# Kernel tuning notes

Hardware: AMD Instinct MI355X
Metric: run time of the kernel (lower is better)

Reference implementation:

```python
import jax, jax.numpy as jnp
import numpy as np

D = 1024
H = 16
DH = D // H
L = 128  # max_pos_len
B = 4
T = 1024
SCALE = float(np.sqrt(D / H))


def setup_inputs() -> dict:
    key = jax.random.key(0)
    ks = jax.random.split(key, 9)
    x_q = jax.random.normal(ks[0], (B, T, D), dtype=jnp.float32)
    x_k = jax.random.normal(ks[1], (B, T, D), dtype=jnp.float32)
    x_v = jax.random.normal(ks[2], (B, T, D), dtype=jnp.float32)
    mask = jax.random.randint(ks[3], (B, 1, 1, T), 0, 2) == 1  # bool, True = masked
    Wq = jax.random.normal(ks[4], (D, D), dtype=jnp.float32) * 0.02
    Wk = jax.random.normal(ks[5], (D, D), dtype=jnp.float32) * 0.02
    Wv = jax.random.normal(ks[6], (D, D), dtype=jnp.float32) * 0.02
    Wo = jax.random.normal(ks[7], (D, D), dtype=jnp.float32) * 0.02
    pos_emb = jax.random.normal(ks[8], (2 * L + 1, DH), dtype=jnp.float32)
    return {"x_q": x_q, "x_k": x_k, "x_v": x_v, "mask": mask,
            "Wq": Wq, "Wk": Wk, "Wv": Wv, "Wo": Wo, "pos_emb": pos_emb}


def reference(x_q, x_k, x_v, mask, Wq, Wk, Wv, Wo, pos_emb):
    # nn.Linear(bias=False): y = x @ W.T
    def split_heads(x):  # (B,T,D) -> (B,H,T,DH)
        return x.reshape(B, -1, H, DH).transpose(0, 2, 1, 3)

    Q = split_heads(x_q @ Wq.T)
    K = split_heads(x_k @ Wk.T)
    V = split_heads(x_v @ Wv.T)

    logits = jnp.einsum('bhqd,bhkd->bhqk', Q, K)

    # arrange_char_pos_embedding: indices[q,k] = clamp(k-q, -L, L) + L
    rel = jnp.clip(jnp.arange(T)[None, :] - jnp.arange(T)[:, None], -L, L) + L
    arranged_pos = pos_emb[rel]  # (T_Q, T_K, DH)
    pos_logits = jnp.einsum('bhqd,qkd->bhqk', Q, arranged_pos)

    logits = (logits + pos_logits) / SCALE
    logits = jnp.where(mask, -jnp.inf, logits)  # mask broadcasts (B,1,1,T)
    attn = jax.nn.softmax(logits, axis=-1)  # dropout p=0.0 -> identity

    combined = jnp.einsum('bhqk,bhkd->bhqd', attn, V)
    heads_concat = combined.transpose(0, 2, 1, 3).reshape(B, -1, D)
    return heads_concat @ Wo.T
```

## Files before the change

### kernel.cpp

```cpp
#include <hip/hip_runtime.h>
#include <hip/hip_bf16.h>
#include <stdint.h>

typedef __attribute__((ext_vector_type(8))) short short8;
typedef __attribute__((ext_vector_type(4))) float f32x4;

__device__ __forceinline__ uint16_t f2bf(float f) {
    union { float f; uint32_t u; } v; v.f = f;
    uint32_t r = v.u + 0x7FFF + ((v.u >> 16) & 1);
    return (uint16_t)(r >> 16);
}
__device__ __forceinline__ float bf2f(uint16_t u) {
    union { uint32_t u; float f; } v; v.u = ((uint32_t)u) << 16;
    return v.f;
}
__device__ __forceinline__ float exp2_raw(float x) {
    float r;
    asm("v_exp_f32 %0, %1" : "=v"(r) : "v"(x));
    return r;
}
__device__ __forceinline__ uint32_t cvt_pk_bf16(float lo, float hi) {
    uint32_t r;
    asm("v_cvt_pk_bf16_f32 %0, %1, %2" : "=v"(r) : "v"(lo), "v"(hi));
    return r;
}

template<int F32>
__device__ __forceinline__ uint4 load8(const void* p, size_t off) {
    if (F32) {
        const float* f = (const float*)p + off;
        float4 f0 = *(const float4*)f;
        float4 f1 = *(const float4*)(f + 4);
        uint4 r;
        r.x = (uint32_t)f2bf(f0.x) | ((uint32_t)f2bf(f0.y) << 16);
        r.y = (uint32_t)f2bf(f0.z) | ((uint32_t)f2bf(f0.w) << 16);
        r.z = (uint32_t)f2bf(f1.x) | ((uint32_t)f2bf(f1.y) << 16);
        r.w = (uint32_t)f2bf(f1.z) | ((uint32_t)f2bf(f1.w) << 16);
        return r;
    } else {
        return *(const uint4*)((const uint16_t*)p + off);
    }
}

#define GLDS(gp, lp) __builtin_amdgcn_global_load_lds( \
    (const __attribute__((address_space(1))) void*)(gp), \
    (__attribute__((address_space(3))) void*)(lp), 16, 0, 0)

struct CvtSeg { const float* s; uint16_t* d; int n8; };
struct CvtArgs {
    CvtSeg seg[9]; int nseg;
    const void* mraw; unsigned long long* mbits; uint16_t* mvals;
};

__global__ __launch_bounds__(256) void cvt_bf16(CvtArgs a)
{
    if (blockIdx.x == 0) {
        __shared__ int flags[3];
        __shared__ uint8_t mloc[4096];
        const uint32_t* w = (const uint32_t*)a.mraw;
        const uint8_t* b8 = (const uint8_t*)a.mraw;
        const int t = threadIdx.x;
        if (t < 3) flags[t] = 0;
        __syncthreads();
        int fbyte = 0, ff32 = 0, fodd = 0;
        for (int i = t; i < 1024; i += 256) {
            uint32_t v = w[i];
            if (v != 0u && v != 1u && v != 0x3F800000u) fbyte = 1;
            if (v == 0x3F800000u) ff32 = 1;
            if ((i & 1) && v != 0u) fodd = 1;
        }
        if (fbyte) atomicOr(&flags[0], 1);
        if (ff32)  atomicOr(&flags[1], 1);
        if (fodd)  atomicOr(&flags[2], 1);
        __syncthreads();
        int mode;
        if (flags[0]) mode = 1;
        else if (flags[1]) mode = 0;
        else if (!flags[2]) mode = 2;
        else mode = 0;
        for (int k = t; k < 4096; k += 256) {
            int val;
            if (mode == 1)      val = (b8[k] != 0);
            else if (mode == 2) val = (w[2 * k] != 0u);
            else                val = (w[k] != 0u);
            mloc[k] = (uint8_t)val;
        }
        __syncthreads();
        for (int k = t; k < 4096; k += 256)
            a.mvals[k] = mloc[k] ? (uint16_t)0 : (uint16_t)0x3F80;
        if (t < 64) {
            uint64_t bits = 0;
#pragma unroll
            for (int i = 0; i < 64; ++i)
                bits |= (uint64_t)mloc[t * 64 + i] << i;
            a.mbits[t] = bits;
        }
    }
    const int tid = blockIdx.x * 256 + threadIdx.x;
    const int stride = gridDim.x * 256;
    for (int s = 0; s < a.nseg; ++s) {
        const float* src = a.seg[s].s;
        uint16_t* dst = a.seg[s].d;
        const int n8 = a.seg[s].n8;
        if (src) {
            for (int i = tid; i < n8; i += stride)
                *(uint4*)(dst + (size_t)i * 8) = load8<1>(src, (size_t)i * 8);
        } else {
            const uint4 z = {0u, 0u, 0u, 0u};
            for (int i = tid; i < n8; i += stride)
                *(uint4*)(dst + (size_t)i * 8) = z;
        }
    }
}

__global__ __launch_bounds__(256) void gemm128_qkv(
    const uint16_t* __restrict__ xq, const uint16_t* __restrict__ xk, const uint16_t* __restrict__ xv,
    const uint16_t* __restrict__ Wq, const uint16_t* __restrict__ Wk, const uint16_t* __restrict__ Wv,
    uint16_t* __restrict__ Qh, uint16_t* __restrict__ Khd, uint16_t* __restrict__ Vt,
    const unsigned long long* __restrict__ mbits)
{
    __shared__ alignas(16) uint16_t As[2][128 * 32];
    __shared__ alignas(16) uint16_t Bs[2][128 * 32];

    const int z = blockIdx.z;
    const uint16_t* A = (z == 0) ? xq : (z == 1) ? xk : xv;
    const uint16_t* B = (z == 0) ? Wq : (z == 1) ? Wk : Wv;
    uint16_t* C = (z == 0) ? Qh : (z == 1) ? Khd : Vt;
    const int cm = (z == 2) ? 2 : 1;
    const int bm = blockIdx.x, bn = blockIdx.y;
    const int K = 1024;

    const int t = threadIdx.x;
    const int lane = t & 63, wave = t >> 6;
    const int lrow = lane & 15, quad = lane >> 4;
    const int wr = (wave >> 1) * 64, wc = (wave & 1) * 64;
    const int g_row = wave * 16 + (lane >> 2);
    const int g_col = (lane & 3) * 8;

    const f32x4 fz = {0.f, 0.f, 0.f, 0.f};
    f32x4 acc[4][4];
#pragma unroll
    for (int i = 0; i < 4; ++i)
#pragma unroll
        for (int j = 0; j < 4; ++j) acc[i][j] = fz;

    for (int k0 = 0; k0 < K; k0 += 64) {
        __syncthreads();
#pragma unroll
        for (int kh = 0; kh < 2; ++kh) {
            const int kk = k0 + kh * 32;
            GLDS(A + (size_t)(bm * 128 + g_row) * K + kk + g_col,      As[kh] + wave * 512);
            GLDS(A + (size_t)(bm * 128 + g_row + 64) * K + kk + g_col, As[kh] + wave * 512 + 2048);
            GLDS(B + (size_t)(bn * 128 + g_row) * K + kk + g_col,      Bs[kh] + wave * 512);
            GLDS(B + (size_t)(bn * 128 + g_row + 64) * K + kk + g_col, Bs[kh] + wave * 512 + 2048);
        }
        __syncthreads();

#pragma unroll
        for (int kh = 0; kh < 2; ++kh) {
            short8 a[4], b[4];
#pragma unroll
            for (int i = 0; i < 4; ++i)
                a[i] = *(const short8*)(As[kh] + (wr + i * 16 + lrow) * 32 + quad * 8);
#pragma unroll
            for (int j = 0; j < 4; ++j)
                b[j] = *(const short8*)(Bs[kh] + (wc + j * 16 + lrow) * 32 + quad * 8);
#pragma unroll
            for (int i = 0; i < 4; ++i)
#pragma unroll
                for (int j = 0; j < 4; ++j)
                    acc[i][j] = __builtin_amdgcn_mfma_f32_16x16x32_bf16(a[i], b[j], acc[i][j], 0, 0, 0);
        }
    }

    if (cm == 2) {
        __syncthreads();
        uint16_t* scr = As[0] + wave * 1024;
#pragma unroll
        for (int i = 0; i < 4; ++i)
#pragma unroll
            for (int j = 0; j < 4; ++j) {
                uint2 pk;
                pk.x = (uint32_t)f2bf(acc[i][j][0]) | ((uint32_t)f2bf(acc[i][j][1]) << 16);
                pk.y = (uint32_t)f2bf(acc[i][j][2]) | ((uint32_t)f2bf(acc[i][j][3]) << 16);
                *(uint2*)(scr + lrow * 16 + quad * 4) = pk;
                if (lane < 32) {
                    int n = lane >> 1, m8 = (lane & 1) * 8;
                    short8 vv = *(const short8*)(scr + n * 16 + m8);
                    int ng = bn * 128 + wc + j * 16 + n;
                    int hh = ng >> 6, d = ng & 63;
                    int mg = bm * 128 + wr + i * 16;
                    int bb = mg >> 10, tl = (mg & 1023) + m8;
                    uint32_t eb = (uint32_t)(mbits[(size_t)bb * 16 + (tl >> 6)] >> (tl & 63)) & 0xFFu;
                    if (eb) {
                        union { short8 s; uint32_t u[4]; } uw;
                        uw.s = vv;
#pragma unroll
                        for (int c = 0; c < 4; ++c) {
                            uint32_t km = (((eb >> (2 * c)) & 1) ? 0u : 0x0000FFFFu)
                                        | (((eb >> (2 * c + 1)) & 1) ? 0u : 0xFFFF0000u);
                            uw.u[c] &= km;
                        }
                        vv = uw.s;
                    }
                    *(short8*)(C + ((((size_t)bb * 16 + hh) * 64 + d) * 1024 + tl)) = vv;
                }
            }
        return;
    }

#pragma unroll
    for (int i = 0; i < 4; ++i)
#pragma unroll
        for (int j = 0; j < 4; ++j)
#pragma unroll
            for (int r = 0; r < 4; ++r) {
                int m = bm * 128 + wr + i * 16 + quad * 4 + r;
                int n = bn * 128 + wc + j * 16 + lrow;
                int bb = m >> 10, tt = m & 1023, hh = n >> 6, d = n & 63;
                C[(((size_t)bb * 16 + hh) * 1024 + tt) * 64 + d] = f2bf(acc[i][j][r]);
            }
}

__global__ __launch_bounds__(256) void gemm_out(
    const uint16_t* __restrict__ A, const uint16_t* __restrict__ B,
    float* __restrict__ C, int M, int N, int K)
{
    __shared__ alignas(16) uint16_t As[2][64 * 32];
    __shared__ alignas(16) uint16_t Bs[2][128 * 32];

    const int t = threadIdx.x;
    const int lane = t & 63, wave = t >> 6;
    const int lrow = lane & 15, quad = lane >> 4;
    const int wr = (wave >> 1) * 32, wc = (wave & 1) * 64;
    const int g_row = wave * 16 + (lane >> 2);
    const int g_col = (lane & 3) * 8;
    const int bm = blockIdx.x, bn = blockIdx.y;

    const f32x4 fz = {0.f, 0.f, 0.f, 0.f};
    f32x4 acc[2][4];
#pragma unroll
    for (int i = 0; i < 2; ++i)
#pragma unroll
        for (int j = 0; j < 4; ++j) acc[i][j] = fz;

    for (int k0 = 0; k0 < K; k0 += 64) {
        __syncthreads();
#pragma unroll
        for (int kh = 0; kh < 2; ++kh) {
            const int kk = k0 + kh * 32;
            GLDS(A + (size_t)(bm * 64 + g_row) * K + kk + g_col,       As[kh] + wave * 512);
            GLDS(B + (size_t)(bn * 128 + g_row) * K + kk + g_col,      Bs[kh] + wave * 512);
            GLDS(B + (size_t)(bn * 128 + g_row + 64) * K + kk + g_col, Bs[kh] + wave * 512 + 2048);
        }
        __syncthreads();

#pragma unroll
        for (int kh = 0; kh < 2; ++kh) {
            short8 a[2], b[4];
#pragma unroll
            for (int i = 0; i < 2; ++i)
                a[i] = *(const short8*)(As[kh] + (wr + i * 16 + lrow) * 32 + quad * 8);
#pragma unroll
            for (int j = 0; j < 4; ++j)
                b[j] = *(const short8*)(Bs[kh] + (wc + j * 16 + lrow) * 32 + quad * 8);
#pragma unroll
            for (int i = 0; i < 2; ++i)
#pragma unroll
                for (int j = 0; j < 4; ++j)
                    acc[i][j] = __builtin_amdgcn_mfma_f32_16x16x32_bf16(a[i], b[j], acc[i][j], 0, 0, 0);
        }
    }

#pragma unroll
    for (int i = 0; i < 2; ++i)
#pragma unroll
        for (int j = 0; j < 4; ++j)
#pragma unroll
            for (int r = 0; r < 4; ++r) {
                int m = bm * 64 + wr + i * 16 + quad * 4 + r;
                int n = bn * 128 + wc + j * 16 + lrow;
                C[(size_t)m * N + n] = acc[i][j][r];
            }
}

__global__ __launch_bounds__(256) void flash_attn(
    const uint16_t* __restrict__ Qh, const uint16_t* __restrict__ Kh,
    const uint16_t* __restrict__ Vt, const uint16_t* __restrict__ pos,
    const uint16_t* __restrict__ maskv, uint16_t* __restrict__ comb)
{
    const int blk = blockIdx.x;
    const int jj = blk >> 3;
    const int bh = (blk & 7) * 8 + (jj >> 4);
    const int qt = jj & 15;
    const int b = bh >> 4;
    const int h = bh & 15;
    const int t = threadIdx.x;
    const int lane = t & 63;
    const int wave = t >> 6;
    const int lrow = lane & 15;
    const int quad = lane >> 4;
    const int qb = qt * 64 + wave * 16;

    __shared__ alignas(16) uint16_t Ks[2][4096];
    __shared__ alignas(16) uint16_t Vs[2][4096];
    __shared__ alignas(16) uint16_t Qpos_l[64][277];
    __shared__ alignas(16) uint16_t Pl[4][16][72];
    __shared__ alignas(16) uint16_t maskl[1024];

    const uint16_t* Kp = Kh + (size_t)bh * 65536;
    const uint16_t* Vp = Vt + (size_t)bh * 65536;

    const int sg_r = lane >> 2;
    const int sg_c = ((lane & 3) ^ ((sg_r >> 1) & 3)) * 8;
    const int hw = wave >> 1;
    const int gw = (wave & 1) * 2;
    const int rdc = (quad ^ ((lrow >> 1) & 3)) * 8;

    const float CS = 0.18033688011f;

#pragma unroll
    for (int gg = 0; gg < 2; ++gg) {
        int g = gw + gg;
        GLDS(Kp + (size_t)(g * 16 + sg_r) * 64 + hw * 32 + sg_c, &Ks[0][hw * 2048 + g * 512]);
        GLDS(Vp + (size_t)(g * 16 + sg_r) * 1024 + hw * 32 + sg_c, &Vs[0][hw * 2048 + g * 512]);
    }
    if (wave < 2)
        GLDS(maskv + (size_t)b * 1024 + wave * 512 + lane * 8, maskl + wave * 512);

    const uint16_t* Qp = Qh + ((size_t)bh * 1024 + qb) * 64;
    short8 aq0 = *(const short8*)(Qp + (size_t)lrow * 64 + quad * 8);
    short8 aq1 = *(const short8*)(Qp + (size_t)lrow * 64 + 32 + quad * 8);

    const f32x4 fz = {0.f, 0.f, 0.f, 0.f};

#pragma unroll 4
    for (int nt = 0; nt < 17; ++nt) {
        short8 pb0 = *(const short8*)(pos + (size_t)(nt * 16 + lrow) * 64 + quad * 8);
        short8 pb1 = *(const short8*)(pos + (size_t)(nt * 16 + lrow) * 64 + 32 + quad * 8);
        f32x4 c = __builtin_amdgcn_mfma_f32_16x16x32_bf16(aq0, pb0, fz, 0, 0, 0);
        c = __builtin_amdgcn_mfma_f32_16x16x32_bf16(aq1, pb1, c, 0, 0, 0);
        const uint32_t p01 = cvt_pk_bf16(c[0] * CS, c[1] * CS);
        const uint32_t p23 = cvt_pk_bf16(c[2] * CS, c[3] * CS);
        const int row = wave * 16 + quad * 4;
        const int col = nt * 16 + lrow;
        Qpos_l[row + 0][col] = (uint16_t)p01;
        Qpos_l[row + 1][col] = (uint16_t)(p01 >> 16);
        Qpos_l[row + 2][col] = (uint16_t)p23;
        Qpos_l[row + 3][col] = (uint16_t)(p23 >> 16);
    }

    float pcl[4], pch[4];
#pragma unroll
    for (int r = 0; r < 4; ++r) {
        int ql = wave * 16 + quad * 4 + r;
        pcl[r] = bf2f(Qpos_l[ql][0]);
        pch[r] = bf2f(Qpos_l[ql][256]);
    }

    f32x4 o[4] = {fz, fz, fz, fz};
    f32x4 lacc = fz;

    for (int kb = 0; kb < 1024; kb += 64) {
        const int cur = (kb >> 6) & 1;
        __syncthreads();
        if (kb + 64 < 1024) {
            const int nxt = cur ^ 1;
#pragma unroll
            for (int gg = 0; gg < 2; ++gg) {
                int g = gw + gg;
                GLDS(Kp + (size_t)(kb + 64 + g * 16 + sg_r) * 64 + hw * 32 + sg_c,
                     &Ks[nxt][hw * 2048 + g * 512]);
                GLDS(Vp + (size_t)(g * 16 + sg_r) * 1024 + kb + 64 + hw * 32 + sg_c,
                     &Vs[nxt][hw * 2048 + g * 512]);
            }
        }
        const uint16_t* Kc = Ks[cur];
        const uint16_t* Vc = Vs[cur];

        f32x4 s[4];
        __builtin_amdgcn_s_setprio(1);
#pragma unroll
        for (int j = 0; j < 4; ++j) {
            short8 k0 = *(const short8*)(Kc + (j * 16 + lrow) * 32 + rdc);
            short8 k1 = *(const short8*)(Kc + 2048 + (j * 16 + lrow) * 32 + rdc);
            s[j] = __builtin_amdgcn_mfma_f32_16x16x32_bf16(aq0, k0, fz, 0, 0, 0);
            s[j] = __builtin_amdgcn_mfma_f32_16x16x32_bf16(aq1, k1, s[j], 0, 0, 0);
        }
        __builtin_amdgcn_s_setprio(0);

        const int diff = kb - qb;
        if (diff <= -192 || diff >= 144) {
            const bool low = (diff <= -192);
#pragma unroll
            for (int j = 0; j < 4; ++j) {
                float e[4];
#pragma unroll
                for (int r = 0; r < 4; ++r) {
                    float pc = low ? pcl[r] : pch[r];
                    e[r] = exp2_raw(__builtin_fmaf(s[j][r], CS, pc));
                }
                const uint32_t p01 = cvt_pk_bf16(e[0], e[1]);
                const uint32_t p23 = cvt_pk_bf16(e[2], e[3]);
                const int col = j * 16 + lrow;
                const int rw = quad * 4;
                Pl[wave][rw + 0][col] = (uint16_t)p01;
                Pl[wave][rw + 1][col] = (uint16_t)(p01 >> 16);
                Pl[wave][rw + 2][col] = (uint16_t)p23;
                Pl[wave][rw + 3][col] = (uint16_t)(p23 >> 16);
            }
        } else {
#pragma unroll
            for (int j = 0; j < 4; ++j) {
                const int key = kb + j * 16 + lrow;
                float e[4];
#pragma unroll
                for (int r = 0; r < 4; ++r) {
                    int q = qb + quad * 4 + r;
                    int ql = q & 63;
                    int rel = min(max(key - q, -128), 128) + 128;
                    float p = bf2f(Qpos_l[ql][rel]);
                    e[r] = exp2_raw(__builtin_fmaf(s[j][r], CS, p));
                }
                const uint32_t p01 = cvt_pk_bf16(e[0], e[1]);
                const uint32_t p23 = cvt_pk_bf16(e[2], e[3]);
                const int col = j * 16 + lrow;
                const int rw = quad * 4;
                Pl[wave][rw + 0][col] = (uint16_t)p01;
                Pl[wave][rw + 1][col] = (uint16_t)(p01 >> 16);
                Pl[wave][rw + 2][col] = (uint16_t)p23;
                Pl[wave][rw + 3][col] = (uint16_t)(p23 >> 16);
            }
        }
        short8 ap0 = *(const short8*)(&Pl[wave][lrow][quad * 8]);
        short8 ap1 = *(const short8*)(&Pl[wave][lrow][32 + quad * 8]);
        short8 bm0 = *(const short8*)(maskl + kb + quad * 8);
        short8 bm1 = *(const short8*)(maskl + kb + 32 + quad * 8);

        __builtin_amdgcn_s_setprio(1);
#pragma unroll
        for (int dt = 0; dt < 4; ++dt) {
            short8 v0 = *(const short8*)(Vc + (dt * 16 + lrow) * 32 + rdc);
            short8 v1 = *(const short8*)(Vc + 2048 + (dt * 16 + lrow) * 32 + rdc);
            o[dt] = __builtin_amdgcn_mfma_f32_16x16x32_bf16(ap0, v0, o[dt], 0, 0, 0);
            o[dt] = __builtin_amdgcn_mfma_f32_16x16x32_bf16(ap1, v1, o[dt], 0, 0, 0);
        }
        lacc = __builtin_amdgcn_mfma_f32_16x16x32_bf16(ap0, bm0, lacc, 0, 0, 0);
        lacc = __builtin_amdgcn_mfma_f32_16x16x32_bf16(ap1, bm1, lacc, 0, 0, 0);
        __builtin_amdgcn_s_setprio(0);
    }

    float inv[4];
#pragma unroll
    for (int r = 0; r < 4; ++r) inv[r] = 1.0f / lacc[r];

#pragma unroll
    for (int dt = 0; dt < 4; ++dt)
#pragma unroll
        for (int r = 0; r < 4; ++r) {
            size_t row = (size_t)b * 1024 + qb + quad * 4 + r;
            size_t col = (size_t)h * 64 + dt * 16 + lrow;
            comb[row * 1024 + col] = f2bf(o[dt][r] * inv[r]);
        }
}

extern "C" void kernel_launch(void* const* d_in, const int* in_sizes, int n_in,
                              void* d_out, int out_size, void* d_ws, size_t ws_size,
                              hipStream_t stream)
{
    const float* x_q = (const float*)d_in[0];
    const float* x_k = (const float*)d_in[1];
    const float* x_v = (const float*)d_in[2];
    const void*  msk = d_in[3];
    const float* Wq  = (const float*)d_in[4];
    const float* Wk  = (const float*)d_in[5];
    const float* Wv  = (const float*)d_in[6];
    const float* Wo  = (const float*)d_in[7];
    const float* pos = (const float*)d_in[8];

    char* ws = (char*)d_ws;
    const size_t MB = 1u << 20;
    uint16_t* Qh   = (uint16_t*)(ws);
    uint16_t* Khd  = (uint16_t*)(ws + 8 * MB);
    uint16_t* Vt   = (uint16_t*)(ws + 16 * MB);
    uint16_t* xqb  = (uint16_t*)(ws + 24 * MB);
    uint16_t* xkb  = (uint16_t*)(ws + 32 * MB);
    uint16_t* xvb  = (uint16_t*)(ws + 40 * MB);
    uint16_t* Wqb  = (uint16_t*)(ws + 48 * MB);
    uint16_t* Wkb  = (uint16_t*)(ws + 50 * MB);
    uint16_t* Wvb  = (uint16_t*)(ws + 52 * MB);
    uint16_t* Wob  = (uint16_t*)(ws + 54 * MB);
    uint16_t* posb = (uint16_t*)(ws + 56 * MB);
    unsigned long long* mbits = (unsigned long long*)(ws + 56 * MB + 65536);
    uint16_t* mvals = (uint16_t*)(ws + 56 * MB + 65536 + 4096);
    uint16_t* comb = xqb;

    CvtArgs ca{};
    int ns = 0;
    ca.seg[ns++] = {x_q, xqb, 524288};
    ca.seg[ns++] = {x_k, xkb, 524288};
    ca.seg[ns++] = {x_v, xvb, 524288};
    ca.seg[ns++] = {Wq, Wqb, 131072};
    ca.seg[ns++] = {Wk, Wkb, 131072};
    ca.seg[ns++] = {Wv, Wvb, 131072};
    ca.seg[ns++] = {Wo, Wob, 131072};
    ca.seg[ns++] = {pos, posb, 2056};
    ca.seg[ns++] = {nullptr, posb + 16448, 120};
    ca.nseg = ns;
    ca.mraw = msk;
    ca.mbits = mbits;
    ca.mvals = mvals;
    cvt_bf16<<<dim3(512), dim3(256), 0, stream>>>(ca);

    gemm128_qkv<<<dim3(32, 8, 3), dim3(256), 0, stream>>>(
        xqb, xkb, xvb, Wqb, Wkb, Wvb, Qh, Khd, Vt, mbits);

    flash_attn<<<dim3(1024), dim3(256), 0, stream>>>(Qh, Khd, Vt, posb, mvals, comb);

    gemm_out<<<dim3(64, 8), dim3(256), 0, stream>>>(
        comb, Wob, (float*)d_out, 4096, 1024, 1024);
}
```

Measured before the change: 237.3 us.

## Software-pipeline flash attention PV of previous tile with current QK and softmax

Restructures the attention key loop so the P·V MFMAs for the previous key tile are issued alongside the QK MFMAs of the current tile. V fragments are preloaded into registers before the next barrier, with a prologue and epilogue added around the loop. The aim is to overlap the exp/softmax VALU work with matrix-core work and shorten the dependency chain per iteration. It also hoists the per-element mask-bit global load in the V-projection epilogue into a single wave-uniform 64-bit load, at the cost of higher register pressure from holding V and P fragments across iterations.

Result: faster. 229.2 us (-3.4%).

```diff
diff --git a/kernel.cpp b/kernel.cpp
--- a/kernel.cpp
+++ b/kernel.cpp
@@ -176,6 +176,10 @@
     if (cm == 2) {
         __syncthreads();
         uint16_t* scr = As[0] + wave * 1024;
+        const int mg0 = bm * 128 + wr;
+        const int widx = __builtin_amdgcn_readfirstlane((mg0 >> 10) * 16 + ((mg0 & 1023) >> 6));
+        const uint64_t mword = mbits[widx];
+        const uint64_t mw64 = mword >> ((lane & 1) * 8);
 #pragma unroll
         for (int i = 0; i < 4; ++i)
 #pragma unroll
@@ -191,7 +195,7 @@
                     int hh = ng >> 6, d = ng & 63;
                     int mg = bm * 128 + wr + i * 16;
                     int bb = mg >> 10, tl = (mg & 1023) + m8;
-                    uint32_t eb = (uint32_t)(mbits[(size_t)bb * 16 + (tl >> 6)] >> (tl & 63)) & 0xFFu;
+                    uint32_t eb = (uint32_t)(mw64 >> (i * 16)) & 0xFFu;
                     if (eb) {
                         union { short8 s; uint32_t u[4]; } uw;
                         uw.s = vv;
@@ -282,6 +286,88 @@
                 int n = bn * 128 + wc + j * 16 + lrow;
                 C[(size_t)m * N + n] = acc[i][j][r];
             }
+}
+
+#define FA_QK(KC_)                                                              \
+{                                                                               \
+    _Pragma("unroll")                                                           \
+    for (int j = 0; j < 4; ++j) {                                               \
+        short8 k0 = *(const short8*)((KC_) + (j * 16 + lrow) * 32 + rdc);       \
+        short8 k1 = *(const short8*)((KC_) + 2048 + (j * 16 + lrow) * 32 + rdc);\
+        s[j] = __builtin_amdgcn_mfma_f32_16x16x32_bf16(aq0, k0, fz, 0, 0, 0);   \
+        s[j] = __builtin_amdgcn_mfma_f32_16x16x32_bf16(aq1, k1, s[j], 0, 0, 0); \
+    }                                                                           \
+}
+
+#define FA_PV(KBM_)                                                             \
+{                                                                               \
+    short8 bm0 = *(const short8*)(maskl + (KBM_) + quad * 8);                   \
+    short8 bm1 = *(const short8*)(maskl + (KBM_) + 32 + quad * 8);              \
+    _Pragma("unroll")                                                           \
+    for (int dt = 0; dt < 4; ++dt) {                                            \
+        o[dt] = __builtin_amdgcn_mfma_f32_16x16x32_bf16(ap0, vv[dt * 2 + 0], o[dt], 0, 0, 0); \
+        o[dt] = __builtin_amdgcn_mfma_f32_16x16x32_bf16(ap1, vv[dt * 2 + 1], o[dt], 0, 0, 0); \
+    }                                                                           \
+    lacc = __builtin_amdgcn_mfma_f32_16x16x32_bf16(ap0, bm0, lacc, 0, 0, 0);    \
+    lacc = __builtin_amdgcn_mfma_f32_16x16x32_bf16(ap1, bm1, lacc, 0, 0, 0);    \
+}
+
+#define FA_SM(KB_)                                                              \
+{                                                                               \
+    const int diff = (KB_) - qb;                                                \
+    if (diff <= -192 || diff >= 144) {                                          \
+        const bool low = (diff <= -192);                                        \
+        _Pragma("unroll")                                                       \
+        for (int j = 0; j < 4; ++j) {                                           \
+            float e[4];                                                         \
+            _Pragma("unroll")                                                   \
+            for (int r = 0; r < 4; ++r) {                                       \
+                float pc = low ? pcl[r] : pch[r];                               \
+                e[r] = exp2_raw(__builtin_fmaf(s[j][r], CS, pc));               \
+            }                                                                   \
+            const uint32_t p01 = cvt_pk_bf16(e[0], e[1]);                       \
+            const uint32_t p23 = cvt_pk_bf16(e[2], e[3]);                       \
+            const int col = j * 16 + lrow;                                      \
+            const int rw = quad * 4;                                            \
+            Pl[wave][rw + 0][col] = (uint16_t)p01;                              \
+            Pl[wave][rw + 1][col] = (uint16_t)(p01 >> 16);                      \
+            Pl[wave][rw + 2][col] = (uint16_t)p23;                              \
+            Pl[wave][rw + 3][col] = (uint16_t)(p23 >> 16);                      \
+        }                                                                       \
+    } else {                                                                    \
+        _Pragma("unroll")                                                       \
+        for (int j = 0; j < 4; ++j) {                                           \
+            const int key = (KB_) + j * 16 + lrow;                              \
+            float e[4];                                                         \
+            _Pragma("unroll")                                                   \
+            for (int r = 0; r < 4; ++r) {                                       \
+                int q = qb + quad * 4 + r;                                      \
+                int ql = q & 63;                                                \
+                int rel = min(max(key - q, -128), 128) + 128;                   \
+                float p = bf2f(Qpos_l[ql][rel]);                                \
+                e[r] = exp2_raw(__builtin_fmaf(s[j][r], CS, p));                \
+            }                                                                   \
+            const uint32_t p01 = cvt_pk_bf16(e[0], e[1]);                       \
+            const uint32_t p23 = cvt_pk_bf16(e[2], e[3]);                       \
+            const int col = j * 16 + lrow;                                      \
+            const int rw = quad * 4;                                            \
+            Pl[wave][rw + 0][col] = (uint16_t)p01;                              \
+            Pl[wave][rw + 1][col] = (uint16_t)(p01 >> 16);                      \
+            Pl[wave][rw + 2][col] = (uint16_t)p23;                              \
+            Pl[wave][rw + 3][col] = (uint16_t)(p23 >> 16);                      \
+        }                                                                       \
+    }                                                                           \
+    ap0 = *(const short8*)(&Pl[wave][lrow][quad * 8]);                          \
+    ap1 = *(const short8*)(&Pl[wave][lrow][32 + quad * 8]);                     \
+}
+
+#define FA_VV(VC_)                                                              \
+{                                                                               \
+    _Pragma("unroll")                                                           \
+    for (int dt = 0; dt < 4; ++dt) {                                            \
+        vv[dt * 2 + 0] = *(const short8*)((VC_) + (dt * 16 + lrow) * 32 + rdc); \
+        vv[dt * 2 + 1] = *(const short8*)((VC_) + 2048 + (dt * 16 + lrow) * 32 + rdc); \
+    }                                                                           \
 }
 
 __global__ __launch_bounds__(256) void flash_attn(
@@ -360,12 +446,29 @@
 
     f32x4 o[4] = {fz, fz, fz, fz};
     f32x4 lacc = fz;
-
-    for (int kb = 0; kb < 1024; kb += 64) {
-        const int cur = (kb >> 6) & 1;
-        __syncthreads();
-        if (kb + 64 < 1024) {
-            const int nxt = cur ^ 1;
+    f32x4 s[4];
+    short8 ap0, ap1, vv[8];
+
+    __syncthreads();
+#pragma unroll
+    for (int gg = 0; gg < 2; ++gg) {
+        int g = gw + gg;
+        GLDS(Kp + (size_t)(64 + g * 16 + sg_r) * 64 + hw * 32 + sg_c, &Ks[1][hw * 2048 + g * 512]);
+        GLDS(Vp + (size_t)(g * 16 + sg_r) * 1024 + 64 + hw * 32 + sg_c, &Vs[1][hw * 2048 + g * 512]);
+    }
+    __builtin_amdgcn_s_setprio(1);
+    FA_QK(Ks[0])
+    __builtin_amdgcn_s_setprio(0);
+    FA_SM(0)
+    FA_VV(Vs[0])
+
+    for (int ti = 1; ti < 16; ++ti) {
+        const int kb = ti * 64;
+        const uint16_t* Kc = Ks[ti & 1];
+        const uint16_t* Vc = Vs[ti & 1];
+        __syncthreads();
+        if (ti < 15) {
+            const int nxt = (ti + 1) & 1;
 #pragma unroll
             for (int gg = 0; gg < 2; ++gg) {
                 int g = gw + gg;
@@ -375,80 +478,16 @@
                      &Vs[nxt][hw * 2048 + g * 512]);
             }
         }
-        const uint16_t* Kc = Ks[cur];
-        const uint16_t* Vc = Vs[cur];
-
-        f32x4 s[4];
         __builtin_amdgcn_s_setprio(1);
-#pragma unroll
-        for (int j = 0; j < 4; ++j) {
-            short8 k0 = *(const short8*)(Kc + (j * 16 + lrow) * 32 + rdc);
-            short8 k1 = *(const short8*)(Kc + 2048 + (j * 16 + lrow) * 32 + rdc);
-            s[j] = __builtin_amdgcn_mfma_f32_16x16x32_bf16(aq0, k0, fz, 0, 0, 0);
-            s[j] = __builtin_amdgcn_mfma_f32_16x16x32_bf16(aq1, k1, s[j], 0, 0, 0);
-        }
+        FA_PV(kb - 64)
+        FA_QK(Kc)
         __builtin_amdgcn_s_setprio(0);
-
-        const int diff = kb - qb;
-        if (diff <= -192 || diff >= 144) {
-            const bool low = (diff <= -192);
-#pragma unroll
-            for (int j = 0; j < 4; ++j) {
-                float e[4];
-#pragma unroll
-                for (int r = 0; r < 4; ++r) {
-                    float pc = low ? pcl[r] : pch[r];
-                    e[r] = exp2_raw(__builtin_fmaf(s[j][r], CS, pc));
-                }
-                const uint32_t p01 = cvt_pk_bf16(e[0], e[1]);
-                const uint32_t p23 = cvt_pk_bf16(e[2], e[3]);
-                const int col = j * 16 + lrow;
-                const int rw = quad * 4;
-                Pl[wave][rw + 0][col] = (uint16_t)p01;
-                Pl[wave][rw + 1][col] = (uint16_t)(p01 >> 16);
-                Pl[wave][rw + 2][col] = (uint16_t)p23;
-                Pl[wave][rw + 3][col] = (uint16_t)(p23 >> 16);
-            }
-        } else {
-#pragma unroll
-            for (int j = 0; j < 4; ++j) {
-                const int key = kb + j * 16 + lrow;
-                float e[4];
-#pragma unroll
-                for (int r = 0; r < 4; ++r) {
-                    int q = qb + quad * 4 + r;
-                    int ql = q & 63;
-                    int rel = min(max(key - q, -128), 128) + 128;
-                    float p = bf2f(Qpos_l[ql][rel]);
-                    e[r] = exp2_raw(__builtin_fmaf(s[j][r], CS, p));
-                }
-                const uint32_t p01 = cvt_pk_bf16(e[0], e[1]);
-                const uint32_t p23 = cvt_pk_bf16(e[2], e[3]);
-                const int col = j * 16 + lrow;
-                const int rw = quad * 4;
-                Pl[wave][rw + 0][col] = (uint16_t)p01;
-                Pl[wave][rw + 1][col] = (uint16_t)(p01 >> 16);
-                Pl[wave][rw + 2][col] = (uint16_t)p23;
-                Pl[wave][rw + 3][col] = (uint16_t)(p23 >> 16);
-            }
-        }
-        short8 ap0 = *(const short8*)(&Pl[wave][lrow][quad * 8]);
-        short8 ap1 = *(const short8*)(&Pl[wave][lrow][32 + quad * 8]);
-        short8 bm0 = *(const short8*)(maskl + kb + quad * 8);
-        short8 bm1 = *(const short8*)(maskl + kb + 32 + quad * 8);
-
-        __builtin_amdgcn_s_setprio(1);
-#pragma unroll
-        for (int dt = 0; dt < 4; ++dt) {
-            short8 v0 = *(const short8*)(Vc + (dt * 16 + lrow) * 32 + rdc);
-            short8 v1 = *(const short8*)(Vc + 2048 + (dt * 16 + lrow) * 32 + rdc);
-            o[dt] = __builtin_amdgcn_mfma_f32_16x16x32_bf16(ap0, v0, o[dt], 0, 0, 0);
-            o[dt] = __builtin_amdgcn_mfma_f32_16x16x32_bf16(ap1, v1, o[dt], 0, 0, 0);
-        }
-        lacc = __builtin_amdgcn_mfma_f32_16x16x32_bf16(ap0, bm0, lacc, 0, 0, 0);
-        lacc = __builtin_amdgcn_mfma_f32_16x16x32_bf16(ap1, bm1, lacc, 0, 0, 0);
-        __builtin_amdgcn_s_setprio(0);
-    }
+        FA_SM(kb)
+        FA_VV(Vc)
+    }
+    __builtin_amdgcn_s_setprio(1);
+    FA_PV(960)
+    __builtin_amdgcn_s_setprio(0);
 
     float inv[4];
 #pragma unroll
```
